# Optimization experiments

Hardware: AMD Instinct MI355X
Metric: run time of the kernel (lower is better)

## Reference

```python
import jax, jax.numpy as jnp
import numpy as np

B, T, D, H = 2, 2048, 1024, 16
STD = 0.02

def setup_inputs() -> dict:
    key = jax.random.key(0)
    ks = jax.random.split(key, 5)
    x = jax.random.normal(ks[0], (B, T, D), dtype=jnp.float32)
    Wq = jax.random.normal(ks[1], (D, D), dtype=jnp.float32) * STD
    Wk = jax.random.normal(ks[2], (D, D), dtype=jnp.float32) * STD
    Wv = jax.random.normal(ks[3], (D, D), dtype=jnp.float32) * STD
    Wo = jax.random.normal(ks[4], (D, D), dtype=jnp.float32) * STD
    z = jnp.zeros((D,), dtype=jnp.float32)
    return {"x": x, "Wq": Wq, "bq": z, "Wk": Wk, "bk": z, "Wv": Wv, "bv": z, "Wo": Wo, "bo": z}

def _split(t, h):
    b, s, dm = t.shape
    return t.reshape(b, s, h, dm // h).transpose(0, 2, 1, 3)  # (B,h,T,d)

def reference(x, Wq, bq, Wk, bk, Wv, bv, Wo, bo):
    h = H
    # linear projections (nn.Linear: y = x @ W^T + b)
    q = _split(x @ Wq.T + bq, h)
    k = _split(x @ Wk.T + bk, h)
    v = _split(x @ Wv.T + bv, h)
    d_k = k.shape[-1]
    # scaled dot-product similarities (B,h,T,T)
    sim = jnp.einsum("bhqd,bhkd->bhqk", q, k) / jnp.sqrt(jnp.float32(d_k))
    # causal mask: upper triangle (excluding diag) filled with -inf
    Tq = sim.shape[-1]
    causal = jnp.tril(jnp.ones((Tq, Tq), dtype=bool))
    sim = jnp.where(causal, sim, -jnp.inf)
    attn = jax.nn.softmax(sim, axis=-1)
    ctx = jnp.einsum("bhqk,bhkd->bhqd", attn, v)  # (B,h,T,d)
    ctx = ctx.transpose(0, 2, 1, 3).reshape(x.shape[0], x.shape[1], -1)  # (B,T,D)
    return ctx @ Wo.T + bo
```

## Files before the change

### kernel.cpp

```cpp
#include <hip/hip_runtime.h>
#include <hip/hip_bf16.h>


typedef __attribute__((ext_vector_type(8))) short bf16x8;
typedef __attribute__((ext_vector_type(4))) float f32x4;
typedef __attribute__((ext_vector_type(4))) short s16x4;

#define QSCALE 0.18033688011f

__device__ __forceinline__ int sniff_f32(const void* p) {
    const unsigned short* u = (const unsigned short*)p;
    int c = 0;
    for (int i = 0; i < 256; ++i) {
        int e = (u[i] >> 7) & 0xFF;
        c += (e >= 0x90) ? 1 : 0;
    }
    return c > 8;
}

__device__ __forceinline__ void async_copy16(const void* g, void* l) {
    __builtin_amdgcn_global_load_lds(
        (const __attribute__((address_space(1))) void*)g,
        (__attribute__((address_space(3))) void*)l, 16, 0, 0);
}

struct Cvt { const void* src; __hip_bfloat16* dst; int n; };
struct CvtPack { Cvt a[9]; };

__global__ __launch_bounds__(256) void cvt_bf16(CvtPack pk) {
    const Cvt c = pk.a[blockIdx.y];
    const int f32 = sniff_f32(c.src);
    const int stride = gridDim.x * 256 * 8;
    for (int idx = (blockIdx.x * 256 + threadIdx.x) * 8; idx < c.n; idx += stride) {
        if (f32) {
            const float* s = (const float*)c.src + idx;
            f32x4 a0 = *(const f32x4*)s;
            f32x4 a1 = *(const f32x4*)(s + 4);
            union { __hip_bfloat16 h[8]; bf16x8 v; } u;
#pragma unroll
            for (int e = 0; e < 4; e++) u.h[e]     = (__hip_bfloat16)a0[e];
#pragma unroll
            for (int e = 0; e < 4; e++) u.h[4 + e] = (__hip_bfloat16)a1[e];
            *(bf16x8*)&c.dst[idx] = u.v;
        } else {
            *(bf16x8*)&c.dst[idx] = *(const bf16x8*)((const __hip_bfloat16*)c.src + idx);
        }
    }
}

template <int MODE>
__device__ __forceinline__ void gemm_async_body(
    const __hip_bfloat16* __restrict__ A, const __hip_bfloat16* __restrict__ W,
    const __hip_bfloat16* __restrict__ bias, void* __restrict__ C,
    int M, int N, int K, int bm, int bn, float outscale,
    __hip_bfloat16* sA, __hip_bfloat16* sB)
{
    const int tid  = threadIdx.x;
    const int wave = tid >> 6;
    const int lane = tid & 63;
    const int quad = lane >> 4;
    const int l15  = lane & 15;
    const int wr   = wave >> 1;
    const int wc   = wave & 1;

    const int srow = wave * 16 + (lane >> 2);
    const int scol = (lane & 3) * 8;
    const __hip_bfloat16* gA0 = A + (size_t)(bm + srow) * K + scol;
    const __hip_bfloat16* gB0 = W + (size_t)(bn + srow) * K + scol;
    __hip_bfloat16* sA0 = sA + wave * 512;
    __hip_bfloat16* sB0 = sB + wave * 512;

    f32x4 acc[4][4];
#pragma unroll
    for (int i = 0; i < 4; i++)
#pragma unroll
        for (int j = 0; j < 4; j++) acc[i][j] = (f32x4)0.0f;

    for (int k0 = 0; k0 < K; k0 += 32) {
        __syncthreads();
#pragma unroll
        for (int r = 0; r < 2; r++) {
            async_copy16(gA0 + (size_t)r * 64 * K + k0, sA0 + r * 2048);
            async_copy16(gB0 + (size_t)r * 64 * K + k0, sB0 + r * 2048);
        }
        __syncthreads();

        bf16x8 af[4], bf[4];
#pragma unroll
        for (int i = 0; i < 4; i++)
            af[i] = *(const bf16x8*)&sA[(wr * 64 + i * 16 + l15) * 32 + quad * 8];
#pragma unroll
        for (int j = 0; j < 4; j++)
            bf[j] = *(const bf16x8*)&sB[(wc * 64 + j * 16 + l15) * 32 + quad * 8];
#pragma unroll
        for (int i = 0; i < 4; i++)
#pragma unroll
            for (int j = 0; j < 4; j++)
                acc[i][j] = __builtin_amdgcn_mfma_f32_16x16x32_bf16(af[i], bf[j], acc[i][j], 0, 0, 0);
    }

    float bv[4];
#pragma unroll
    for (int j = 0; j < 4; j++)
        bv[j] = (float)bias[bn + wc * 64 + j * 16 + l15];

    if (MODE == 2) {
        __hip_bfloat16* VTo = (__hip_bfloat16*)C;
#pragma unroll
        for (int i = 0; i < 4; i++) {
            int tglob = bm + wr * 64 + i * 16 + quad * 4;
            int bb = tglob >> 11, tt = tglob & 2047;
#pragma unroll
            for (int j = 0; j < 4; j++) {
                int d = bn + wc * 64 + j * 16 + l15;
                int hh = d >> 6, dh = d & 63;
                union { __hip_bfloat16 e[4]; s16x4 v; } u;
#pragma unroll
                for (int r = 0; r < 4; r++)
                    u.e[r] = (__hip_bfloat16)(acc[i][j][r] + bv[j]);
                *(s16x4*)&VTo[(((size_t)bb * 16 + hh) * 64 + dh) * 2048 + tt] = u.v;
            }
        }
    } else {
#pragma unroll
        for (int i = 0; i < 4; i++) {
#pragma unroll
            for (int j = 0; j < 4; j++) {
                int col = bn + wc * 64 + j * 16 + l15;
#pragma unroll
                for (int r = 0; r < 4; r++) {
                    int row = bm + wr * 64 + i * 16 + quad * 4 + r;
                    float v = (acc[i][j][r] + bv[j]) * outscale;
                    if (MODE == 1) ((float*)C)[(size_t)row * N + col] = v;
                    else ((__hip_bfloat16*)C)[(size_t)row * N + col] = (__hip_bfloat16)v;
                }
            }
        }
    }
}

__global__ __launch_bounds__(256, 2) void qkv_gemm(
    const __hip_bfloat16* __restrict__ x,
    const __hip_bfloat16* __restrict__ Wq, const __hip_bfloat16* __restrict__ bq, __hip_bfloat16* __restrict__ Q,
    const __hip_bfloat16* __restrict__ Wk, const __hip_bfloat16* __restrict__ bk, __hip_bfloat16* __restrict__ Kb,
    const __hip_bfloat16* __restrict__ Wv, const __hip_bfloat16* __restrict__ bv, __hip_bfloat16* __restrict__ VT,
    int M, int N, int K)
{
    __shared__ __hip_bfloat16 sA[128 * 32];
    __shared__ __hip_bfloat16 sB[128 * 32];
    if (blockIdx.z == 0)
        gemm_async_body<0>(x, Wq, bq, Q, M, N, K, blockIdx.x * 128, blockIdx.y * 128, QSCALE, sA, sB);
    else if (blockIdx.z == 1)
        gemm_async_body<0>(x, Wk, bk, Kb, M, N, K, blockIdx.x * 128, blockIdx.y * 128, 1.0f, sA, sB);
    else
        gemm_async_body<2>(x, Wv, bv, VT, M, N, K, blockIdx.x * 128, blockIdx.y * 128, 1.0f, sA, sB);
}

template <bool OF32>
__device__ __forceinline__ void gemm64_body(
    const __hip_bfloat16* __restrict__ A, const __hip_bfloat16* __restrict__ W,
    const __hip_bfloat16* __restrict__ bias, void* __restrict__ C,
    int M, int N, int K, int bm, int bn,
    __hip_bfloat16* sA, __hip_bfloat16* sB)
{
    const int tid  = threadIdx.x;
    const int wave = tid >> 6;
    const int lane = tid & 63;
    const int quad = lane >> 4;
    const int l15  = lane & 15;

    const int srow = wave * 16 + (lane >> 2);
    const int scol = (lane & 3) * 8;
    const __hip_bfloat16* gA0 = A + (size_t)(bm + srow) * K + scol;
    const __hip_bfloat16* gB0 = W + (size_t)(bn + srow) * K + scol;
    __hip_bfloat16* sA0 = sA + wave * 512;
    __hip_bfloat16* sB0 = sB + wave * 512;

    f32x4 acc[4][2];
#pragma unroll
    for (int i = 0; i < 4; i++)
#pragma unroll
        for (int j = 0; j < 2; j++) acc[i][j] = (f32x4)0.0f;

    for (int k0 = 0; k0 < K; k0 += 32) {
        __syncthreads();
        async_copy16(gA0 + k0, sA0);
#pragma unroll
        for (int r = 0; r < 2; r++)
            async_copy16(gB0 + (size_t)r * 64 * K + k0, sB0 + r * 2048);
        __syncthreads();

        bf16x8 af[4], bf[2];
#pragma unroll
        for (int i = 0; i < 4; i++)
            af[i] = *(const bf16x8*)&sA[(i * 16 + l15) * 32 + quad * 8];
#pragma unroll
        for (int j = 0; j < 2; j++)
            bf[j] = *(const bf16x8*)&sB[(wave * 32 + j * 16 + l15) * 32 + quad * 8];
#pragma unroll
        for (int i = 0; i < 4; i++)
#pragma unroll
            for (int j = 0; j < 2; j++)
                acc[i][j] = __builtin_amdgcn_mfma_f32_16x16x32_bf16(af[i], bf[j], acc[i][j], 0, 0, 0);
    }

    float bv[2];
#pragma unroll
    for (int j = 0; j < 2; j++)
        bv[j] = (float)bias[bn + wave * 32 + j * 16 + l15];
#pragma unroll
    for (int i = 0; i < 4; i++) {
#pragma unroll
        for (int j = 0; j < 2; j++) {
            int col = bn + wave * 32 + j * 16 + l15;
#pragma unroll
            for (int r = 0; r < 4; r++) {
                int row = bm + i * 16 + quad * 4 + r;
                float v = acc[i][j][r] + bv[j];
                if (OF32) ((float*)C)[(size_t)row * N + col] = v;
                else      ((__hip_bfloat16*)C)[(size_t)row * N + col] = (__hip_bfloat16)v;
            }
        }
    }
}

__global__ __launch_bounds__(256, 2) void out_gemm(
    const __hip_bfloat16* __restrict__ A, const __hip_bfloat16* __restrict__ W,
    const __hip_bfloat16* __restrict__ bias, const void* __restrict__ origW,
    void* __restrict__ C, int M, int N, int K)
{
    __shared__ __hip_bfloat16 sA[64 * 32];
    __shared__ __hip_bfloat16 sB[128 * 32];
    __shared__ int f32flag;
    if (threadIdx.x == 0) f32flag = sniff_f32(origW);
    __syncthreads();
    if (f32flag)
        gemm64_body<true>(A, W, bias, C, M, N, K, blockIdx.x * 64, blockIdx.y * 128, sA, sB);
    else
        gemm64_body<false>(A, W, bias, C, M, N, K, blockIdx.x * 64, blockIdx.y * 128, sA, sB);
}

#define PAD 68

__global__ __launch_bounds__(256, 2) void attn_causal(
    const __hip_bfloat16* __restrict__ Q,
    const __hip_bfloat16* __restrict__ K,
    const __hip_bfloat16* __restrict__ VT,
    __hip_bfloat16* __restrict__ O,
    int T, int D, int H)
{
    __shared__ __hip_bfloat16 sK[2][64 * PAD];
    __shared__ __hip_bfloat16 sVT[2][64 * PAD];
    __shared__ __hip_bfloat16 sPA[4][32 * PAD];

    const int tid  = threadIdx.x;
    const int wave = tid >> 6;
    const int lane = tid & 63;
    const int quad = lane >> 4;
    const int l15  = lane & 15;

    const int NT = T >> 7;
    const int qt = blockIdx.z ? (NT - 1 - (int)blockIdx.x) : (int)blockIdx.x;
    const int h  = blockIdx.y;
    const int b  = blockIdx.z;
    const size_t headoff = (size_t)b * T * D + (size_t)h * 64;
    const size_t vtoff   = ((size_t)b * H + h) * 64 * (size_t)T;

    const int nkt = 2 * qt + 2;
    const int myrowmax = qt * 128 + wave * 32 + 31;

    bf16x8 qfrag[2][2];
#pragma unroll
    for (int g = 0; g < 2; g++)
#pragma unroll
        for (int kk = 0; kk < 2; kk++)
            qfrag[g][kk] = *(const bf16x8*)&Q[headoff +
                (size_t)(qt * 128 + wave * 32 + g * 16 + l15) * D + kk * 32 + quad * 8];

    f32x4 acc_o[2][4];
#pragma unroll
    for (int g = 0; g < 2; g++)
#pragma unroll
        for (int j = 0; j < 4; j++) acc_o[g][j] = (f32x4)0.0f;
    float lacc[2] = {0.f, 0.f};

    const int srow = tid >> 3;
    const int sc8  = (tid & 7) * 8;

    bf16x8 pk[2], pv[2];
#pragma unroll
    for (int u = 0; u < 2; u++) {
        int row = srow + u * 32;
        pk[u] = *(const bf16x8*)&K[headoff + (size_t)row * D + sc8];
        pv[u] = *(const bf16x8*)&VT[vtoff + (size_t)row * T + sc8];
    }
#pragma unroll
    for (int u = 0; u < 2; u++) {
        int row = srow + u * 32;
        *(bf16x8*)&sK[0][row * PAD + sc8]  = pk[u];
        *(bf16x8*)&sVT[0][row * PAD + sc8] = pv[u];
    }
    if (nkt > 1) {
#pragma unroll
        for (int u = 0; u < 2; u++) {
            int row = srow + u * 32;
            pk[u] = *(const bf16x8*)&K[headoff + (size_t)(64 + row) * D + sc8];
            pv[u] = *(const bf16x8*)&VT[vtoff + (size_t)row * T + 64 + sc8];
        }
    }
    __syncthreads();

    for (int kt = 0; kt < nkt; ++kt) {
        const int cur = kt & 1;

        if (kt + 1 < nkt) {
#pragma unroll
            for (int u = 0; u < 2; u++) {
                int row = srow + u * 32;
                *(bf16x8*)&sK[1 - cur][row * PAD + sc8]  = pk[u];
                *(bf16x8*)&sVT[1 - cur][row * PAD + sc8] = pv[u];
            }
            if (kt + 2 < nkt) {
#pragma unroll
                for (int u = 0; u < 2; u++) {
                    int row = srow + u * 32;
                    pk[u] = *(const bf16x8*)&K[headoff + (size_t)((kt + 2) * 64 + row) * D + sc8];
                    pv[u] = *(const bf16x8*)&VT[vtoff + (size_t)row * T + (kt + 2) * 64 + sc8];
                }
            }
        }

        if (kt * 64 <= myrowmax) {
            bf16x8 kfrag[2][4], vfrag[2][4];
#pragma unroll
            for (int kk = 0; kk < 2; kk++)
#pragma unroll
                for (int j = 0; j < 4; j++) {
                    kfrag[kk][j] = *(const bf16x8*)&sK[cur][(j * 16 + l15) * PAD + kk * 32 + quad * 8];
                    vfrag[kk][j] = *(const bf16x8*)&sVT[cur][(j * 16 + l15) * PAD + kk * 32 + quad * 8];
                }

#pragma unroll
            for (int g = 0; g < 2; g++) {
                const int qbase = qt * 128 + wave * 32 + g * 16;
                f32x4 st[4];
#pragma unroll
                for (int j = 0; j < 4; j++) st[j] = (f32x4)0.0f;
#pragma unroll
                for (int kk = 0; kk < 2; kk++)
#pragma unroll
                    for (int j = 0; j < 4; j++)
                        st[j] = __builtin_amdgcn_mfma_f32_16x16x32_bf16(
                            kfrag[kk][j], qfrag[g][kk], st[j], 0, 0, 0);

                if (kt * 64 + 63 > qbase) {
                    const int q = qbase + l15;
#pragma unroll
                    for (int j = 0; j < 4; j++) {
                        int keyb = kt * 64 + j * 16 + quad * 4;
#pragma unroll
                        for (int r = 0; r < 4; r++)
                            if (keyb + r > q) st[j][r] = -1e30f;
                    }
                }

#pragma unroll
                for (int j = 0; j < 4; j++) {
                    union { __hip_bfloat16 e[4]; s16x4 v; } u;
#pragma unroll
                    for (int r = 0; r < 4; r++) {
                        float p = exp2f(st[j][r]);
                        lacc[g] += p;
                        u.e[r] = (__hip_bfloat16)p;
                    }
                    *(s16x4*)&sPA[wave][(g * 16 + l15) * PAD + j * 16 + quad * 4] = u.v;
                }
            }
#pragma unroll
            for (int g = 0; g < 2; g++)
#pragma unroll
                for (int kk = 0; kk < 2; kk++) {
                    bf16x8 a = *(const bf16x8*)&sPA[wave][(g * 16 + l15) * PAD + kk * 32 + quad * 8];
#pragma unroll
                    for (int j = 0; j < 4; j++)
                        acc_o[g][j] = __builtin_amdgcn_mfma_f32_16x16x32_bf16(
                            a, vfrag[kk][j], acc_o[g][j], 0, 0, 0);
                }
        }

        __syncthreads();
    }

#pragma unroll
    for (int g = 0; g < 2; g++) {
        lacc[g] += __shfl_xor(lacc[g], 16, 64);
        lacc[g] += __shfl_xor(lacc[g], 32, 64);
    }

#pragma unroll
    for (int g = 0; g < 2; g++)
#pragma unroll
        for (int r = 0; r < 4; r++) {
            float linv = 1.0f / __shfl(lacc[g], quad * 4 + r, 64);
            int row = qt * 128 + wave * 32 + g * 16 + quad * 4 + r;
#pragma unroll
            for (int j = 0; j < 4; j++) {
                int col = j * 16 + l15;
                O[headoff + (size_t)row * D + col] = (__hip_bfloat16)(acc_o[g][j][r] * linv);
            }
        }
}

extern "C" void kernel_launch(void* const* d_in, const int* in_sizes, int n_in,
                              void* d_out, int out_size, void* d_ws, size_t ws_size,
                              hipStream_t stream) {
    const int Bb = 2, T = 2048, D = 1024, H = 16;
    const int M = Bb * T;

    __hip_bfloat16* w = (__hip_bfloat16*)d_ws;
    __hip_bfloat16* Q   = w;
    __hip_bfloat16* Kb  = Q   + (size_t)M * D;
    __hip_bfloat16* VT  = Kb  + (size_t)M * D;
    __hip_bfloat16* ctx = VT  + (size_t)M * D;
    __hip_bfloat16* xb  = ctx + (size_t)M * D;
    __hip_bfloat16* Wqb = xb  + (size_t)M * D;
    __hip_bfloat16* Wkb = Wqb + (size_t)D * D;
    __hip_bfloat16* Wvb = Wkb + (size_t)D * D;
    __hip_bfloat16* Wob = Wvb + (size_t)D * D;
    __hip_bfloat16* bqb = Wob + (size_t)D * D;
    __hip_bfloat16* bkb = bqb + D;
    __hip_bfloat16* bvb = bkb + D;
    __hip_bfloat16* bob = bvb + D;

    CvtPack pk;
    pk.a[0] = { d_in[0], xb,  M * D };
    pk.a[1] = { d_in[1], Wqb, D * D };
    pk.a[2] = { d_in[2], bqb, D };
    pk.a[3] = { d_in[3], Wkb, D * D };
    pk.a[4] = { d_in[4], bkb, D };
    pk.a[5] = { d_in[5], Wvb, D * D };
    pk.a[6] = { d_in[6], bvb, D };
    pk.a[7] = { d_in[7], Wob, D * D };
    pk.a[8] = { d_in[8], bob, D };

    cvt_bf16<<<dim3(512, 9), 256, 0, stream>>>(pk);
    qkv_gemm<<<dim3(M / 128, D / 128, 3), 256, 0, stream>>>(
        xb, Wqb, bqb, Q, Wkb, bkb, Kb, Wvb, bvb, VT, M, D, D);
    attn_causal<<<dim3(T / 128, H, Bb), 256, 0, stream>>>(Q, Kb, VT, ctx, T, D, H);
    out_gemm<<<dim3(M / 64, D / 128), 256, 0, stream>>>(
        ctx, Wob, bob, d_in[7], d_out, M, D, D);
}
```

Measured before the change: 213.6 us.

## Use one-wave attention blocks loading K/V fragments directly into registers

The causal attention kernel is restructured from 256-thread blocks covering 128 query rows into 64-thread single-wave blocks covering 32 query rows, launched as a 4x larger grid. The shared-memory staging of K and V^T and the per-tile block barriers are removed; each wave loads its MFMA fragments straight from global memory into two register buffers and alternates between them. Query-tile order is flipped by a mix of head and batch to balance the causal workload. In exchange, K/V data is no longer shared across the four waves of a block, so global/L2 traffic rises and register pressure grows.

```diff
diff --git a/kernel.cpp b/kernel.cpp
--- a/kernel.cpp
+++ b/kernel.cpp
@@ -242,32 +242,28 @@
 
 #define PAD 68
 
-__global__ __launch_bounds__(256, 2) void attn_causal(
+__global__ __launch_bounds__(64, 2) void attn_causal(
     const __hip_bfloat16* __restrict__ Q,
     const __hip_bfloat16* __restrict__ K,
     const __hip_bfloat16* __restrict__ VT,
     __hip_bfloat16* __restrict__ O,
     int T, int D, int H)
 {
-    __shared__ __hip_bfloat16 sK[2][64 * PAD];
-    __shared__ __hip_bfloat16 sVT[2][64 * PAD];
-    __shared__ __hip_bfloat16 sPA[4][32 * PAD];
-
-    const int tid  = threadIdx.x;
-    const int wave = tid >> 6;
-    const int lane = tid & 63;
+    __shared__ __hip_bfloat16 sPA[32 * PAD];
+
+    const int lane = threadIdx.x;
     const int quad = lane >> 4;
     const int l15  = lane & 15;
 
-    const int NT = T >> 7;
-    const int qt = blockIdx.z ? (NT - 1 - (int)blockIdx.x) : (int)blockIdx.x;
-    const int h  = blockIdx.y;
-    const int b  = blockIdx.z;
+    const int nti = T >> 5;
+    const int flip = ((blockIdx.y >> 2) ^ blockIdx.z) & 1;
+    const int qi  = flip ? (nti - 1 - (int)blockIdx.x) : (int)blockIdx.x;
+    const int h   = blockIdx.y;
+    const int b   = blockIdx.z;
     const size_t headoff = (size_t)b * T * D + (size_t)h * 64;
     const size_t vtoff   = ((size_t)b * H + h) * 64 * (size_t)T;
 
-    const int nkt = 2 * qt + 2;
-    const int myrowmax = qt * 128 + wave * 32 + 31;
+    const int nkt = (qi >> 1) + 1;
 
     bf16x8 qfrag[2][2];
 #pragma unroll
@@ -275,7 +271,7 @@
 #pragma unroll
         for (int kk = 0; kk < 2; kk++)
             qfrag[g][kk] = *(const bf16x8*)&Q[headoff +
-                (size_t)(qt * 128 + wave * 32 + g * 16 + l15) * D + kk * 32 + quad * 8];
+                (size_t)(qi * 32 + g * 16 + l15) * D + kk * 32 + quad * 8];
 
     f32x4 acc_o[2][4];
 #pragma unroll
@@ -284,111 +280,76 @@
         for (int j = 0; j < 4; j++) acc_o[g][j] = (f32x4)0.0f;
     float lacc[2] = {0.f, 0.f};
 
-    const int srow = tid >> 3;
-    const int sc8  = (tid & 7) * 8;
-
-    bf16x8 pk[2], pv[2];
-#pragma unroll
-    for (int u = 0; u < 2; u++) {
-        int row = srow + u * 32;
-        pk[u] = *(const bf16x8*)&K[headoff + (size_t)row * D + sc8];
-        pv[u] = *(const bf16x8*)&VT[vtoff + (size_t)row * T + sc8];
-    }
-#pragma unroll
-    for (int u = 0; u < 2; u++) {
-        int row = srow + u * 32;
-        *(bf16x8*)&sK[0][row * PAD + sc8]  = pk[u];
-        *(bf16x8*)&sVT[0][row * PAD + sc8] = pv[u];
-    }
-    if (nkt > 1) {
-#pragma unroll
-        for (int u = 0; u < 2; u++) {
-            int row = srow + u * 32;
-            pk[u] = *(const bf16x8*)&K[headoff + (size_t)(64 + row) * D + sc8];
-            pv[u] = *(const bf16x8*)&VT[vtoff + (size_t)row * T + 64 + sc8];
-        }
-    }
-    __syncthreads();
-
-    for (int kt = 0; kt < nkt; ++kt) {
-        const int cur = kt & 1;
-
+    bf16x8 kfA[2][4], vfA[2][4], kfB[2][4], vfB[2][4];
+
+    auto LOAD = [&](int kt, bf16x8 (&kf)[2][4], bf16x8 (&vf)[2][4]) {
+#pragma unroll
+        for (int kk = 0; kk < 2; kk++)
+#pragma unroll
+            for (int j = 0; j < 4; j++) {
+                kf[kk][j] = *(const bf16x8*)&K[headoff +
+                    (size_t)(kt * 64 + j * 16 + l15) * D + kk * 32 + quad * 8];
+                vf[kk][j] = *(const bf16x8*)&VT[vtoff +
+                    (size_t)(j * 16 + l15) * T + kt * 64 + kk * 32 + quad * 8];
+            }
+    };
+
+    auto COMPUTE = [&](int kt, bf16x8 (&kf)[2][4], bf16x8 (&vf)[2][4], bool mask) {
+#pragma unroll
+        for (int g = 0; g < 2; g++) {
+            f32x4 st[4];
+#pragma unroll
+            for (int j = 0; j < 4; j++) st[j] = (f32x4)0.0f;
+#pragma unroll
+            for (int kk = 0; kk < 2; kk++)
+#pragma unroll
+                for (int j = 0; j < 4; j++)
+                    st[j] = __builtin_amdgcn_mfma_f32_16x16x32_bf16(
+                        kf[kk][j], qfrag[g][kk], st[j], 0, 0, 0);
+
+            if (mask) {
+                const int qv = qi * 32 + g * 16 + l15;
+#pragma unroll
+                for (int j = 0; j < 4; j++) {
+                    int keyb = kt * 64 + j * 16 + quad * 4;
+#pragma unroll
+                    for (int r = 0; r < 4; r++)
+                        if (keyb + r > qv) st[j][r] = -1e30f;
+                }
+            }
+
+#pragma unroll
+            for (int j = 0; j < 4; j++) {
+                union { __hip_bfloat16 e[4]; s16x4 v; } u;
+#pragma unroll
+                for (int r = 0; r < 4; r++) {
+                    float p = exp2f(st[j][r]);
+                    lacc[g] += p;
+                    u.e[r] = (__hip_bfloat16)p;
+                }
+                *(s16x4*)&sPA[(g * 16 + l15) * PAD + j * 16 + quad * 4] = u.v;
+            }
+        }
+#pragma unroll
+        for (int g = 0; g < 2; g++)
+#pragma unroll
+            for (int kk = 0; kk < 2; kk++) {
+                bf16x8 a = *(const bf16x8*)&sPA[(g * 16 + l15) * PAD + kk * 32 + quad * 8];
+#pragma unroll
+                for (int j = 0; j < 4; j++)
+                    acc_o[g][j] = __builtin_amdgcn_mfma_f32_16x16x32_bf16(
+                        a, vf[kk][j], acc_o[g][j], 0, 0, 0);
+            }
+    };
+
+    LOAD(0, kfA, vfA);
+    for (int kt = 0; kt < nkt; kt += 2) {
+        if (kt + 1 < nkt) LOAD(kt + 1, kfB, vfB);
+        COMPUTE(kt, kfA, vfA, kt == nkt - 1);
         if (kt + 1 < nkt) {
-#pragma unroll
-            for (int u = 0; u < 2; u++) {
-                int row = srow + u * 32;
-                *(bf16x8*)&sK[1 - cur][row * PAD + sc8]  = pk[u];
-                *(bf16x8*)&sVT[1 - cur][row * PAD + sc8] = pv[u];
-            }
-            if (kt + 2 < nkt) {
-#pragma unroll
-                for (int u = 0; u < 2; u++) {
-                    int row = srow + u * 32;
-                    pk[u] = *(const bf16x8*)&K[headoff + (size_t)((kt + 2) * 64 + row) * D + sc8];
-                    pv[u] = *(const bf16x8*)&VT[vtoff + (size_t)row * T + (kt + 2) * 64 + sc8];
-                }
-            }
-        }
-
-        if (kt * 64 <= myrowmax) {
-            bf16x8 kfrag[2][4], vfrag[2][4];
-#pragma unroll
-            for (int kk = 0; kk < 2; kk++)
-#pragma unroll
-                for (int j = 0; j < 4; j++) {
-                    kfrag[kk][j] = *(const bf16x8*)&sK[cur][(j * 16 + l15) * PAD + kk * 32 + quad * 8];
-                    vfrag[kk][j] = *(const bf16x8*)&sVT[cur][(j * 16 + l15) * PAD + kk * 32 + quad * 8];
-                }
-
-#pragma unroll
-            for (int g = 0; g < 2; g++) {
-                const int qbase = qt * 128 + wave * 32 + g * 16;
-                f32x4 st[4];
-#pragma unroll
-                for (int j = 0; j < 4; j++) st[j] = (f32x4)0.0f;
-#pragma unroll
-                for (int kk = 0; kk < 2; kk++)
-#pragma unroll
-                    for (int j = 0; j < 4; j++)
-                        st[j] = __builtin_amdgcn_mfma_f32_16x16x32_bf16(
-                            kfrag[kk][j], qfrag[g][kk], st[j], 0, 0, 0);
-
-                if (kt * 64 + 63 > qbase) {
-                    const int q = qbase + l15;
-#pragma unroll
-                    for (int j = 0; j < 4; j++) {
-                        int keyb = kt * 64 + j * 16 + quad * 4;
-#pragma unroll
-                        for (int r = 0; r < 4; r++)
-                            if (keyb + r > q) st[j][r] = -1e30f;
-                    }
-                }
-
-#pragma unroll
-                for (int j = 0; j < 4; j++) {
-                    union { __hip_bfloat16 e[4]; s16x4 v; } u;
-#pragma unroll
-                    for (int r = 0; r < 4; r++) {
-                        float p = exp2f(st[j][r]);
-                        lacc[g] += p;
-                        u.e[r] = (__hip_bfloat16)p;
-                    }
-                    *(s16x4*)&sPA[wave][(g * 16 + l15) * PAD + j * 16 + quad * 4] = u.v;
-                }
-            }
-#pragma unroll
-            for (int g = 0; g < 2; g++)
-#pragma unroll
-                for (int kk = 0; kk < 2; kk++) {
-                    bf16x8 a = *(const bf16x8*)&sPA[wave][(g * 16 + l15) * PAD + kk * 32 + quad * 8];
-#pragma unroll
-                    for (int j = 0; j < 4; j++)
-                        acc_o[g][j] = __builtin_amdgcn_mfma_f32_16x16x32_bf16(
-                            a, vfrag[kk][j], acc_o[g][j], 0, 0, 0);
-                }
-        }
-
-        __syncthreads();
+            if (kt + 2 < nkt) LOAD(kt + 2, kfA, vfA);
+            COMPUTE(kt + 1, kfB, vfB, kt + 1 == nkt - 1);
+        }
     }
 
 #pragma unroll
@@ -396,13 +357,12 @@
         lacc[g] += __shfl_xor(lacc[g], 16, 64);
         lacc[g] += __shfl_xor(lacc[g], 32, 64);
     }
-
 #pragma unroll
     for (int g = 0; g < 2; g++)
 #pragma unroll
         for (int r = 0; r < 4; r++) {
             float linv = 1.0f / __shfl(lacc[g], quad * 4 + r, 64);
-            int row = qt * 128 + wave * 32 + g * 16 + quad * 4 + r;
+            int row = qi * 32 + g * 16 + quad * 4 + r;
 #pragma unroll
             for (int j = 0; j < 4; j++) {
                 int col = j * 16 + l15;
@@ -446,7 +406,7 @@
     cvt_bf16<<<dim3(512, 9), 256, 0, stream>>>(pk);
     qkv_gemm<<<dim3(M / 128, D / 128, 3), 256, 0, stream>>>(
         xb, Wqb, bqb, Q, Wkb, bkb, Kb, Wvb, bvb, VT, M, D, D);
-    attn_causal<<<dim3(T / 128, H, Bb), 256, 0, stream>>>(Q, Kb, VT, ctx, T, D, H);
+    attn_causal<<<dim3(T / 32, H, Bb), 64, 0, stream>>>(Q, Kb, VT, ctx, T, D, H);
     out_gemm<<<dim3(M / 64, D / 128), 256, 0, stream>>>(
         ctx, Wob, bob, d_in[7], d_out, M, D, D);
 }
```

New measurement: 233.7 us. +9.4%, slower.
